# Kernel tuning notes

Hardware: AMD Instinct MI355X
Metric: run time of the kernel (lower is better)

Reference implementation:

```python
import jax, jax.numpy as jnp
import numpy as np

N = 131072   # total nodes in batch
E = 524288   # directed edges
B = 2048     # number of graphs
H = 128      # hidden_dim
NF = 30      # node_feature_dim
GF = 4415    # gene_feature_dim
L = 3        # gnn_layers
EPS = 1e-5   # batchnorm eps


def setup_inputs() -> dict:
    key = jax.random.key(0)
    ks = jax.random.split(key, 24)
    rn = lambda k, s, sc=0.05: jax.random.normal(k, s, jnp.float32) * sc
    return {
        "x": jax.random.normal(ks[0], (N, NF), jnp.float32),
        "gene_features": jax.random.normal(ks[1], (B, GF), jnp.float32),
        "edge_index": jax.random.randint(ks[2], (2, E), 0, N),
        "batch": (jnp.arange(N) * B) // N,  # sorted, every graph non-empty
        "W_emb": rn(ks[3], (NF, H)), "b_emb": jnp.zeros((H,), jnp.float32),
        "Wg": rn(ks[4], (L, H, H)), "bg": jnp.zeros((L, H), jnp.float32),
        "bn_gamma": jnp.ones((L, H), jnp.float32), "bn_beta": jnp.zeros((L, H), jnp.float32),
        "Wd1": rn(ks[5], (2 * H, H)), "bd1": jnp.zeros((H,), jnp.float32),
        "Wd2": rn(ks[6], (H, H)), "bd2": jnp.zeros((H,), jnp.float32),
        "Wge1": rn(ks[7], (GF, 256)), "bge1": jnp.zeros((256,), jnp.float32),
        "g_gamma": jnp.ones((256,), jnp.float32), "g_beta": jnp.zeros((256,), jnp.float32),
        "Wge2": rn(ks[8], (256, H)), "bge2": jnp.zeros((H,), jnp.float32),
        "Wh1": rn(ks[9], (2 * H, H)), "bh1": jnp.zeros((H,), jnp.float32),
        "h_gamma": jnp.ones((H,), jnp.float32), "h_beta": jnp.zeros((H,), jnp.float32),
        "Wh2": rn(ks[10], (H, 64)), "bh2": jnp.zeros((64,), jnp.float32),
        "Wh3": rn(ks[11], (64, 1)), "bh3": jnp.zeros((1,), jnp.float32),
    }


def _bn_eval(x, gamma, beta):
    # inference batchnorm with running_mean=0, running_var=1
    return x * (gamma / jnp.sqrt(1.0 + EPS)) + beta


def _gcn_conv(h, W, b, src, dst):
    # PyG GCNConv: add self-loops, symmetric deg normalization, W first, bias after agg
    hw = h @ W                                            # [N,H]
    loop = jnp.arange(N)
    src_a = jnp.concatenate([src, loop])                  # [E+N]
    dst_a = jnp.concatenate([dst, loop])
    deg = jax.ops.segment_sum(jnp.ones((E + N,), hw.dtype), dst_a, num_segments=N)
    dinv = jnp.where(deg > 0, jax.lax.rsqrt(deg), 0.0)
    norm = dinv[src_a] * dinv[dst_a]                      # [E+N]
    msgs = hw[src_a] * norm[:, None]                      # gather [E+N,H]
    out = jax.ops.segment_sum(msgs, dst_a, num_segments=N)
    return out + b


def reference(x, gene_features, edge_index, batch, W_emb, b_emb, Wg, bg, bn_gamma,
              bn_beta, Wd1, bd1, Wd2, bd2, Wge1, bge1, g_gamma, g_beta, Wge2, bge2,
              Wh1, bh1, h_gamma, h_beta, Wh2, bh2, Wh3, bh3):
    src, dst = edge_index[0], edge_index[1]
    h = jax.nn.relu(x @ W_emb + b_emb)                    # [N,H]
    for i in range(L):
        hn = _gcn_conv(h, Wg[i], bg[i], src, dst)
        hn = jax.nn.relu(_bn_eval(hn, bn_gamma[i], bn_beta[i]))
        h = hn if i == 0 else h + hn                      # residual for i>0
    # global mean / max pooling per graph
    counts = jax.ops.segment_sum(jnp.ones((N,), h.dtype), batch, num_segments=B)
    mean_pool = jax.ops.segment_sum(h, batch, num_segments=B) / jnp.maximum(counts, 1.0)[:, None]
    max_pool = jax.ops.segment_max(h, batch, num_segments=B)
    graph_repr = jnp.concatenate([mean_pool, max_pool], axis=1)   # [B,2H]
    drug = jax.nn.relu(graph_repr @ Wd1 + bd1) @ Wd2 + bd2        # [B,H]
    g1 = jax.nn.relu(_bn_eval(gene_features @ Wge1 + bge1, g_gamma, g_beta))
    gene = jax.nn.relu(g1 @ Wge2 + bge2)                          # [B,H]
    comb = jnp.concatenate([drug, gene], axis=1)                  # [B,2H]
    z = jax.nn.relu(_bn_eval(comb @ Wh1 + bh1, h_gamma, h_beta))
    z = jax.nn.relu(z @ Wh2 + bh2)
    return z @ Wh3 + bh3                                          # [B,1]
```

## Files before the change

### kernel.cpp

```cpp
#include <hip/hip_runtime.h>

#define N_NODES 131072
#define E_EDGES 524288
#define B_GR    2048
#define H_DIM   128
#define NF_DIM  30
#define GF_DIM  4415
#define GF_PAD  4416
#define BN_SCALE 0.9999950000374997f

typedef __bf16 bf16x8 __attribute__((ext_vector_type(8)));
typedef float  f32x4  __attribute__((ext_vector_type(4)));
typedef unsigned int uint32;
typedef uint32 u32x4 __attribute__((ext_vector_type(4)));

__device__ __forceinline__ void split2(float x, __bf16& hi, __bf16& lo){
    hi = (__bf16)x;
    lo = (__bf16)(x - (float)hi);
}
__device__ __forceinline__ uint32 bfbits(float x){
    __bf16 h = (__bf16)x;
    return (uint32)__builtin_bit_cast(unsigned short, h);
}
__device__ __forceinline__ float unpack_even(uint32 u){ return __uint_as_float(u<<16); }
__device__ __forceinline__ float unpack_odd (uint32 u){ return __uint_as_float(u & 0xffff0000u); }
__device__ __forceinline__ uint32 pack2(float e, float o){ return bfbits(e) | (bfbits(o)<<16); }


__global__ void k_zero_int(int* __restrict__ p, int n){
    int i = blockIdx.x*256 + threadIdx.x;
    if(i < n) p[i] = 0;
}

__global__ void k_count(const int* __restrict__ dst, int* __restrict__ counts){
    int e = blockIdx.x*256 + threadIdx.x;
    if(e < E_EDGES) atomicAdd(&counts[dst[e]], 1);
}

__global__ void k_scan1(int* __restrict__ counts, int* __restrict__ bsums){
    __shared__ int s[1024];
    int t = threadIdx.x;
    int gi = blockIdx.x*1024 + t;
    int v = counts[gi];
    s[t] = v; __syncthreads();
    for(int off=1; off<1024; off<<=1){
        int x = (t>=off) ? s[t-off] : 0;
        __syncthreads();
        s[t] += x;
        __syncthreads();
    }
    counts[gi] = s[t] - v;
    if(t == 1023) bsums[blockIdx.x] = s[t];
}

__global__ void k_scan2(int* __restrict__ bsums){
    __shared__ int s[128];
    int t = threadIdx.x;
    int v = bsums[t]; s[t] = v; __syncthreads();
    for(int off=1; off<128; off<<=1){
        int x = (t>=off) ? s[t-off] : 0;
        __syncthreads();
        s[t] += x;
        __syncthreads();
    }
    bsums[t] = s[t] - v;
}

__global__ void k_scan3(const int* __restrict__ counts, const int* __restrict__ bsums,
                        int* __restrict__ rowptr){
    int i = blockIdx.x*1024 + threadIdx.x;
    rowptr[i] = counts[i] + bsums[blockIdx.x];
    if(i == 0) rowptr[N_NODES] = E_EDGES;
}

__global__ void k_dinv_cursor(const int* __restrict__ rowptr, float* __restrict__ dinv,
                              int* __restrict__ cursor){
    int n = blockIdx.x*256 + threadIdx.x;
    if(n < N_NODES){
        int a = rowptr[n], b = rowptr[n+1];
        dinv[n] = rsqrtf((float)(b - a) + 1.0f);
        cursor[n] = a;
    }
}

__global__ void k_fill(const int* __restrict__ src, const int* __restrict__ dst,
                       int* __restrict__ cursor, int* __restrict__ csr){
    int e = blockIdx.x*256 + threadIdx.x;
    if(e < E_EDGES){
        int p = atomicAdd(&cursor[dst[e]], 1);
        csr[p] = src[e];
    }
}


__global__ void k_split_weights(const float* __restrict__ Wge1, __bf16* __restrict__ wth,
                                __bf16* __restrict__ wtl,
                                const float* __restrict__ Wg, __bf16* __restrict__ gth,
                                __bf16* __restrict__ gtl,
                                const float* __restrict__ Wemb, __bf16* __restrict__ eth,
                                __bf16* __restrict__ etl){
    unsigned bid = blockIdx.x;
    if(bid < 4416u){
        unsigned idx = bid*256 + threadIdx.x;
        unsigned c = idx / GF_PAD, k = idx - c*GF_PAD;
        float v = (k < GF_DIM) ? Wge1[(size_t)k*256 + c] : 0.f;
        split2(v, wth[idx], wtl[idx]);
    } else if(bid < 4416u + 192u){
        int idx = (bid - 4416u)*256 + threadIdx.x;
        int l = idx >> 14, i = idx & 16383;
        int k = i >> 7, c = i & 127;
        float v = Wg[idx];
        int o = (l << 14) + (c << 7) + k;
        split2(v, gth[o], gtl[o]);
    } else {
        int idx = (bid - 4608u)*256 + threadIdx.x;
        int c = idx >> 5, k = idx & 31;
        float v = (k < NF_DIM) ? Wemb[k*H_DIM + c] : 0.f;
        split2(v, eth[idx], etl[idx]);
    }
}


__global__ __launch_bounds__(256)
void k_emb_mfma(const float* __restrict__ x,
                const __bf16* __restrict__ wth, const __bf16* __restrict__ wtl,
                const float* __restrict__ bias, uint32* __restrict__ Hh2,
                uint32* __restrict__ Hl2){
    __shared__ float sT[4][32*68];
    int wave = threadIdx.x >> 6, lane = threadIdx.x & 63;
    int lr = lane & 15, lq = lane >> 4;
    int rbase = blockIdx.x*128 + wave*32;
    const f32x4 zero4 = {0.f,0.f,0.f,0.f};
    const float* xr0 = x + (size_t)(rbase + lr)*NF_DIM;
    const float* xr1 = x + (size_t)(rbase + 16 + lr)*NF_DIM;
    bf16x8 A0h, A0l, A1h, A1l;
    #pragma unroll
    for(int t=0;t<8;t++){
        int k = lq*8 + t;
        float v0 = (k < NF_DIM) ? xr0[k] : 0.f;
        float v1 = (k < NF_DIM) ? xr1[k] : 0.f;
        __bf16 h, l;
        split2(v0, h, l); A0h[t] = h; A0l[t] = l;
        split2(v1, h, l); A1h[t] = h; A1l[t] = l;
    }
    int orow = lane >> 3;
    int oq   = lane & 7;
    float* sW = sT[wave];
    for(int ph=0; ph<2; ph++){
        #pragma unroll
        for(int cc=0; cc<4; cc++){
            int col = (ph*4+cc)*16 + lr;
            bf16x8 Bh = *(const bf16x8*)(wth + col*32 + lq*8);
            bf16x8 Bl = *(const bf16x8*)(wtl + col*32 + lq*8);
            f32x4 a0 = zero4, a1 = zero4;
            a0 = __builtin_amdgcn_mfma_f32_16x16x32_bf16(A0h, Bh, a0, 0,0,0);
            a0 = __builtin_amdgcn_mfma_f32_16x16x32_bf16(A0l, Bh, a0, 0,0,0);
            a0 = __builtin_amdgcn_mfma_f32_16x16x32_bf16(A0h, Bl, a0, 0,0,0);
            a1 = __builtin_amdgcn_mfma_f32_16x16x32_bf16(A1h, Bh, a1, 0,0,0);
            a1 = __builtin_amdgcn_mfma_f32_16x16x32_bf16(A1l, Bh, a1, 0,0,0);
            a1 = __builtin_amdgcn_mfma_f32_16x16x32_bf16(A1h, Bl, a1, 0,0,0);
            #pragma unroll
            for(int r=0;r<4;r++){
                sW[(lq*4+r)*68 + cc*16 + lr]    = a0[r];
                sW[(16+lq*4+r)*68 + cc*16 + lr] = a1[r];
            }
        }
        __syncthreads();
        int cg = ph*64 + oq*8;
        float bb[8];
        *(float4*)&bb[0] = *(const float4*)(bias + cg);
        *(float4*)&bb[4] = *(const float4*)(bias + cg + 4);
        #pragma unroll
        for(int i=0;i<4;i++){
            int row = i*8 + orow;
            float v[8];
            *(float4*)&v[0] = *(float4*)&sW[row*68 + oq*8];
            *(float4*)&v[4] = *(float4*)&sW[row*68 + oq*8 + 4];
            uint32 oh[4], ol[4];
            #pragma unroll
            for(int p=0;p<4;p++){
                float ve = fmaxf(v[2*p]   + bb[2*p],   0.f);
                float vo = fmaxf(v[2*p+1] + bb[2*p+1], 0.f);
                uint32 he = bfbits(ve), ho = bfbits(vo);
                oh[p] = he | (ho<<16);
                float le = ve - __uint_as_float(he<<16);
                float lo = vo - __uint_as_float(ho<<16);
                ol[p] = pack2(le, lo);
            }
            size_t oidx = (size_t)(rbase + row)*64 + (cg>>1);
            *(uint4*)(Hh2 + oidx) = make_uint4(oh[0],oh[1],oh[2],oh[3]);
            *(uint4*)(Hl2 + oidx) = make_uint4(ol[0],ol[1],ol[2],ol[3]);
        }
        __syncthreads();
    }
}


struct AggMeta {
    int   j0A, cA, j0B, cB;
    float dnA, dnB;
    uint32 shA, slA, shB, slB;
    int   jjA[8], jjB[8];
};

__device__ __forceinline__ void agg_load_meta(AggMeta& m, int nA, int lane,
                                              const int* __restrict__ rowptr,
                                              const float* __restrict__ dinv,
                                              const uint32* __restrict__ Hh2,
                                              const uint32* __restrict__ Hl2){
    int nB = nA + 8;
    int a0 = rowptr[nA], a1 = rowptr[nA+1];
    int b0 = rowptr[nB], b1 = rowptr[nB+1];
    m.j0A = a0; m.cA = a1 - a0;
    m.j0B = b0; m.cB = b1 - b0;
    m.dnA = dinv[nA]; m.dnB = dinv[nB];
    size_t iA = (size_t)nA*64 + lane, iB = (size_t)nB*64 + lane;
    m.shA = Hh2[iA]; m.slA = Hl2[iA];
    m.shB = Hh2[iB]; m.slB = Hl2[iB];
}

__device__ __forceinline__ void agg_load_csr(AggMeta& m, const int* __restrict__ csr){
    int jmA = m.j0A + m.cA - 1;
    int jmB = m.j0B + m.cB - 1;
    #pragma unroll
    for(int t=0;t<8;t++){
        int ia = m.j0A + t; ia = ia > jmA ? jmA : ia;
        int ib = m.j0B + t; ib = ib > jmB ? jmB : ib;
        m.jjA[t] = csr[ia] & (N_NODES-1);
        m.jjB[t] = csr[ib] & (N_NODES-1);
    }
}

__device__ __forceinline__ void agg_pair(AggMeta& cur, AggMeta& nxt, int ii, bool pf,
                                         int rbase, int base16, int lane,
                                         const uint32* __restrict__ Hh2,
                                         const uint32* __restrict__ Hl2,
                                         const float* __restrict__ dinv,
                                         const int* __restrict__ rowptr,
                                         const int* __restrict__ csr,
                                         uint32* __restrict__ AhL,
                                         uint32* __restrict__ AlL){
    uint32 rrA[8], rrB[8];
    float  wwA[8], wwB[8];
    #pragma unroll
    for(int t=0;t<8;t++){
        wwA[t] = (t < cur.cA) ? dinv[cur.jjA[t]] : 0.f;
        rrA[t] = Hh2[(size_t)cur.jjA[t]*64 + lane];
        wwB[t] = (t < cur.cB) ? dinv[cur.jjB[t]] : 0.f;
        rrB[t] = Hh2[(size_t)cur.jjB[t]*64 + lane];
    }
    if(pf){
        agg_load_meta(nxt, rbase + base16 + ii + 1, lane, rowptr, dinv, Hh2, Hl2);
        agg_load_csr(nxt, csr);
    }
    float axA = (unpack_even(cur.shA) + unpack_even(cur.slA)) * cur.dnA;
    float ayA = (unpack_odd(cur.shA)  + unpack_odd(cur.slA))  * cur.dnA;
    float axB = (unpack_even(cur.shB) + unpack_even(cur.slB)) * cur.dnB;
    float ayB = (unpack_odd(cur.shB)  + unpack_odd(cur.slB))  * cur.dnB;
    #pragma unroll
    for(int t=0;t<8;t++){
        axA = fmaf(unpack_even(rrA[t]), wwA[t], axA);
        ayA = fmaf(unpack_odd(rrA[t]),  wwA[t], ayA);
        axB = fmaf(unpack_even(rrB[t]), wwB[t], axB);
        ayB = fmaf(unpack_odd(rrB[t]),  wwB[t], ayB);
    }
    int nb = cur.cA > cur.cB ? cur.cA : cur.cB;
    if(nb > 8){
        int jmA = cur.j0A + cur.cA - 1;
        int jmB = cur.j0B + cur.cB - 1;
        for(int j=8; j<nb; j+=8){
            int jja[8], jjb[8]; float wa[8], wb[8]; uint32 ra[8], rb[8];
            #pragma unroll
            for(int t=0;t<8;t++){
                int ia = cur.j0A + j + t; ia = ia > jmA ? jmA : ia;
                int ib = cur.j0B + j + t; ib = ib > jmB ? jmB : ib;
                jja[t] = csr[ia] & (N_NODES-1);
                jjb[t] = csr[ib] & (N_NODES-1);
            }
            #pragma unroll
            for(int t=0;t<8;t++){
                wa[t] = (j + t < cur.cA) ? dinv[jja[t]] : 0.f;
                ra[t] = Hh2[(size_t)jja[t]*64 + lane];
                wb[t] = (j + t < cur.cB) ? dinv[jjb[t]] : 0.f;
                rb[t] = Hh2[(size_t)jjb[t]*64 + lane];
            }
            #pragma unroll
            for(int t=0;t<8;t++){
                axA = fmaf(unpack_even(ra[t]), wa[t], axA);
                ayA = fmaf(unpack_odd(ra[t]),  wa[t], ayA);
                axB = fmaf(unpack_even(rb[t]), wb[t], axB);
                ayB = fmaf(unpack_odd(rb[t]),  wb[t], ayB);
            }
        }
    }
    axA *= cur.dnA; ayA *= cur.dnA;
    axB *= cur.dnB; ayB *= cur.dnB;
    int rowA = base16 + ii, rowB = rowA + 8;
    uint32 hxA = bfbits(axA), hyA = bfbits(ayA);
    AhL[rowA*68 + lane] = hxA | (hyA<<16);
    AlL[rowA*68 + lane] = pack2(axA - __uint_as_float(hxA<<16),
                                ayA - __uint_as_float(hyA<<16));
    uint32 hxB = bfbits(axB), hyB = bfbits(ayB);
    AhL[rowB*68 + lane] = hxB | (hyB<<16);
    AlL[rowB*68 + lane] = pack2(axB - __uint_as_float(hxB<<16),
                                ayB - __uint_as_float(hyB<<16));
}

__global__ __launch_bounds__(512, 4)
void k_layer(const __bf16* __restrict__ curHh, const __bf16* __restrict__ curHl,
             const float* __restrict__ dinv, const int* __restrict__ rowptr,
             const int* __restrict__ csr,
             const __bf16* __restrict__ Bth, const __bf16* __restrict__ Btl,
             const float* __restrict__ bias, const float* __restrict__ gamma,
             const float* __restrict__ beta,
             uint32* __restrict__ outHh2, uint32* __restrict__ outHl2, int residual){
    __shared__ uint32 smem[8*32*68];
    uint32* AhL = smem;
    uint32* AlL = smem + 128*68;
    int tid  = threadIdx.x;
    int wave = __builtin_amdgcn_readfirstlane(tid >> 6);
    int lane = tid & 63;
    int rbase = blockIdx.x * 128;
    int base16 = wave*16;
    const uint32* Hh2 = (const uint32*)curHh;
    const uint32* Hl2 = (const uint32*)curHl;

    {
        AggMeta m0, m1;
        agg_load_meta(m0, rbase + base16 + 0, lane, rowptr, dinv, Hh2, Hl2);
        agg_load_csr(m0, csr);
        agg_pair(m0, m1, 0, true,  rbase, base16, lane, Hh2, Hl2, dinv, rowptr, csr, AhL, AlL);
        agg_pair(m1, m0, 1, true,  rbase, base16, lane, Hh2, Hl2, dinv, rowptr, csr, AhL, AlL);
        agg_pair(m0, m1, 2, true,  rbase, base16, lane, Hh2, Hl2, dinv, rowptr, csr, AhL, AlL);
        agg_pair(m1, m0, 3, true,  rbase, base16, lane, Hh2, Hl2, dinv, rowptr, csr, AhL, AlL);
        agg_pair(m0, m1, 4, true,  rbase, base16, lane, Hh2, Hl2, dinv, rowptr, csr, AhL, AlL);
        agg_pair(m1, m0, 5, true,  rbase, base16, lane, Hh2, Hl2, dinv, rowptr, csr, AhL, AlL);
        agg_pair(m0, m1, 6, true,  rbase, base16, lane, Hh2, Hl2, dinv, rowptr, csr, AhL, AlL);
        agg_pair(m1, m0, 7, false, rbase, base16, lane, Hh2, Hl2, dinv, rowptr, csr, AhL, AlL);
    }
    __syncthreads();

    int lr = lane & 15, lq = lane >> 4;
    int wr = wave & 3, wc = wave >> 2;
    int r0 = wr*32;
    bf16x8 A0h[4], A0l[4], A1h[4], A1l[4];
    #pragma unroll
    for(int ks=0;ks<4;ks++){
        int u0 = (r0 + lr)*68 + lq*4 + ks*16;
        int u1 = (r0 + 16 + lr)*68 + lq*4 + ks*16;
        A0h[ks] = __builtin_bit_cast(bf16x8, *(const u32x4*)(AhL + u0));
        A0l[ks] = __builtin_bit_cast(bf16x8, *(const u32x4*)(AlL + u0));
        A1h[ks] = __builtin_bit_cast(bf16x8, *(const u32x4*)(AhL + u1));
        A1l[ks] = __builtin_bit_cast(bf16x8, *(const u32x4*)(AlL + u1));
    }
    __syncthreads();

    float* stg = (float*)smem + wave*(32*68);
    const f32x4 zero4 = {0.f,0.f,0.f,0.f};
    #pragma unroll
    for(int cc=0; cc<4; cc++){
        int col = wc*64 + cc*16 + lr;
        f32x4 a0 = zero4, a1 = zero4;
        #pragma unroll
        for(int ks=0;ks<4;ks++){
            bf16x8 Bh = *(const bf16x8*)(Bth + col*H_DIM + ks*32 + lq*8);
            bf16x8 Bl = *(const bf16x8*)(Btl + col*H_DIM + ks*32 + lq*8);
            a0 = __builtin_amdgcn_mfma_f32_16x16x32_bf16(A0h[ks], Bh, a0, 0,0,0);
            a0 = __builtin_amdgcn_mfma_f32_16x16x32_bf16(A0l[ks], Bh, a0, 0,0,0);
            a0 = __builtin_amdgcn_mfma_f32_16x16x32_bf16(A0h[ks], Bl, a0, 0,0,0);
            a1 = __builtin_amdgcn_mfma_f32_16x16x32_bf16(A1h[ks], Bh, a1, 0,0,0);
            a1 = __builtin_amdgcn_mfma_f32_16x16x32_bf16(A1l[ks], Bh, a1, 0,0,0);
            a1 = __builtin_amdgcn_mfma_f32_16x16x32_bf16(A1h[ks], Bl, a1, 0,0,0);
        }
        #pragma unroll
        for(int r=0;r<4;r++){
            stg[(lq*4+r)*68 + cc*16 + lr]    = a0[r];
            stg[(16+lq*4+r)*68 + cc*16 + lr] = a1[r];
        }
    }

    int orow = lane >> 3;
    int oq   = lane & 7;
    int cg = wc*64 + oq*8;
    float bb[8], gg[8], tt[8];
    *(float4*)&bb[0] = *(const float4*)(bias + cg);
    *(float4*)&bb[4] = *(const float4*)(bias + cg + 4);
    *(float4*)&gg[0] = *(const float4*)(gamma + cg);
    *(float4*)&gg[4] = *(const float4*)(gamma + cg + 4);
    *(float4*)&tt[0] = *(const float4*)(beta + cg);
    *(float4*)&tt[4] = *(const float4*)(beta + cg + 4);
    #pragma unroll
    for(int p=0;p<8;p++) gg[p] *= BN_SCALE;
    #pragma unroll
    for(int i=0;i<4;i++){
        int row = i*8 + orow;
        float v[8];
        *(float4*)&v[0] = *(float4*)&stg[row*68 + oq*8];
        *(float4*)&v[4] = *(float4*)&stg[row*68 + oq*8 + 4];
        size_t oidx = (size_t)(rbase + r0 + row)*64 + (cg>>1);
        uint4 oldh = {0,0,0,0}, oldl = {0,0,0,0};
        if(residual){
            oldh = *(const uint4*)(Hh2 + oidx);
            oldl = *(const uint4*)(Hl2 + oidx);
        }
        uint32 ohv[4] = {oldh.x,oldh.y,oldh.z,oldh.w};
        uint32 olv[4] = {oldl.x,oldl.y,oldl.z,oldl.w};
        uint32 oh[4], ol[4];
        #pragma unroll
        for(int p=0;p<4;p++){
            float ve = fmaxf(fmaf(v[2*p]   + bb[2*p],   gg[2*p],   tt[2*p]),   0.f);
            float vo = fmaxf(fmaf(v[2*p+1] + bb[2*p+1], gg[2*p+1], tt[2*p+1]), 0.f);
            if(residual){
                ve += unpack_even(ohv[p]) + unpack_even(olv[p]);
                vo += unpack_odd(ohv[p])  + unpack_odd(olv[p]);
            }
            uint32 he = bfbits(ve), ho = bfbits(vo);
            oh[p] = he | (ho<<16);
            float le = ve - __uint_as_float(he<<16);
            float lo = vo - __uint_as_float(ho<<16);
            ol[p] = pack2(le, lo);
        }
        *(uint4*)(outHh2 + oidx) = make_uint4(oh[0],oh[1],oh[2],oh[3]);
        *(uint4*)(outHl2 + oidx) = make_uint4(ol[0],ol[1],ol[2],ol[3]);
    }
}


__global__ __launch_bounds__(256)
void k_gemm_gf_mfma(const float* __restrict__ Agf,
                    const __bf16* __restrict__ Bth, const __bf16* __restrict__ Btl,
                    float* __restrict__ gpart){
    int rt = blockIdx.x & 31;
    int sp = blockIdx.x >> 5;
    int ks0 = (sp*138) >> 3, ks1 = ((sp+1)*138) >> 3;
    int wave = threadIdx.x >> 6, lane = threadIdx.x & 63;
    int lr = lane & 15, lq = lane >> 4;
    int rbase = rt*64 + (wave & 1)*32;
    int cbase = (wave >> 1)*128;
    const f32x4 zero4 = {0.f,0.f,0.f,0.f};
    f32x4 acc[8][2];
    #pragma unroll
    for(int ct=0;ct<8;ct++){ acc[ct][0] = zero4; acc[ct][1] = zero4; }
    for(int ks=ks0; ks<ks1; ks++){
        int kc = ks*32;
        const float* ar0 = Agf + (size_t)(rbase + lr)*GF_DIM + kc + lq*8;
        const float* ar1 = ar0 + (size_t)16*GF_DIM;
        bf16x8 A0h, A0l, A1h, A1l;
        if(kc + 32 <= GF_DIM){
            #pragma unroll
            for(int t=0;t<8;t++){
                __bf16 h, l;
                split2(ar0[t], h, l); A0h[t] = h; A0l[t] = l;
                split2(ar1[t], h, l); A1h[t] = h; A1l[t] = l;
            }
        } else {
            #pragma unroll
            for(int t=0;t<8;t++){
                int k = kc + lq*8 + t;
                float v0 = 0.f, v1 = 0.f;
                if(k < GF_DIM){ v0 = ar0[t]; v1 = ar1[t]; }
                __bf16 h, l;
                split2(v0, h, l); A0h[t] = h; A0l[t] = l;
                split2(v1, h, l); A1h[t] = h; A1l[t] = l;
            }
        }
        #pragma unroll
        for(int ct=0;ct<8;ct++){
            size_t bo = (size_t)(cbase + ct*16 + lr)*GF_PAD + kc + lq*8;
            bf16x8 Bh = *(const bf16x8*)(Bth + bo);
            bf16x8 Bl = *(const bf16x8*)(Btl + bo);
            acc[ct][0] = __builtin_amdgcn_mfma_f32_16x16x32_bf16(A0h, Bh, acc[ct][0], 0,0,0);
            acc[ct][0] = __builtin_amdgcn_mfma_f32_16x16x32_bf16(A0l, Bh, acc[ct][0], 0,0,0);
            acc[ct][0] = __builtin_amdgcn_mfma_f32_16x16x32_bf16(A0h, Bl, acc[ct][0], 0,0,0);
            acc[ct][1] = __builtin_amdgcn_mfma_f32_16x16x32_bf16(A1h, Bh, acc[ct][1], 0,0,0);
            acc[ct][1] = __builtin_amdgcn_mfma_f32_16x16x32_bf16(A1l, Bh, acc[ct][1], 0,0,0);
            acc[ct][1] = __builtin_amdgcn_mfma_f32_16x16x32_bf16(A1h, Bl, acc[ct][1], 0,0,0);
        }
    }
    float* po = gpart + (size_t)sp*(B_GR*256);
    #pragma unroll
    for(int ct=0;ct<8;ct++)
        #pragma unroll
        for(int s=0;s<2;s++)
            #pragma unroll
            for(int r=0;r<4;r++)
                po[(size_t)(rbase + s*16 + lq*4 + r)*256 + cbase + ct*16 + lr] = acc[ct][s][r];
}

__global__ void k_gene_reduce(const float* __restrict__ gpart, const float* __restrict__ bias,
                              const float* __restrict__ gamma, const float* __restrict__ beta,
                              float* __restrict__ g1){
    int i = blockIdx.x*256 + threadIdx.x;
    int c = i & 255;
    float v = bias[c];
    #pragma unroll
    for(int sp=0;sp<8;sp++) v += gpart[(size_t)sp*(B_GR*256) + i];
    v = fmaf(v, gamma[c]*BN_SCALE, beta[c]);
    g1[i] = fmaxf(v, 0.f);
}


__device__ __forceinline__ void load_w4(const float* __restrict__ W, int off, int tid,
                                        float4* t){
    const float4* s = (const float4*)(W + off);
    t[0] = s[tid];
    t[1] = s[tid + 512];
    t[2] = s[tid + 1024];
    t[3] = s[tid + 1536];
}
__device__ __forceinline__ void write_w4(float* sW, int tid, const float4* t){
    float4* d = (float4*)sW;
    d[tid]        = t[0];
    d[tid + 512]  = t[1];
    d[tid + 1024] = t[2];
    d[tid + 1536] = t[3];
}

__device__ __forceinline__ void dense_stage128(
        const float* __restrict__ W, int nck, const float* sA, int lda,
        float* sO, int ldo, float* sW, int tid, int c, int ga, int gb,
        float bias_c, float gsc, float bsh, int do_relu){
    float4 t[4];
    load_w4(W, 0, tid, t);
    write_w4(sW, tid, t);
    __syncthreads();
    float a0 = bias_c, a1 = bias_c;
    for(int ck=0; ck<nck; ck++){
        if(ck+1 < nck) load_w4(W, (ck+1)*8192, tid, t);
        const float* aga = sA + ga*lda + ck*64;
        const float* agb = sA + gb*lda + ck*64;
        #pragma unroll
        for(int k=0;k<64;k++){
            float w = sW[k*128 + c];
            a0 = fmaf(aga[k], w, a0);
            a1 = fmaf(agb[k], w, a1);
        }
        __syncthreads();
        if(ck+1 < nck){ write_w4(sW, tid, t); __syncthreads(); }
    }
    a0 = fmaf(a0, gsc, bsh);
    a1 = fmaf(a1, gsc, bsh);
    if(do_relu){ a0 = fmaxf(a0, 0.f); a1 = fmaxf(a1, 0.f); }
    sO[ga*ldo + c] = a0;
    sO[gb*ldo + c] = a1;
}

__global__ __launch_bounds__(512)
void k_head(const uint32* __restrict__ Hh2, const uint32* __restrict__ Hl2,
            const float* __restrict__ g1,
            const float* __restrict__ Wd1, const float* __restrict__ bd1,
            const float* __restrict__ Wd2, const float* __restrict__ bd2,
            const float* __restrict__ Wge2, const float* __restrict__ bge2,
            const float* __restrict__ Wh1, const float* __restrict__ bh1,
            const float* __restrict__ h_g, const float* __restrict__ h_b,
            const float* __restrict__ Wh2, const float* __restrict__ bh2,
            const float* __restrict__ Wh3, const float* __restrict__ bh3,
            float* __restrict__ out){
    __shared__ float sPool[8][256];
    __shared__ float sG1[8][256];
    __shared__ float sT1[8][128];
    __shared__ float sComb[8][256];
    __shared__ float sZ[8][128];
    __shared__ float sZ2[8][64];
    __shared__ float sW[8192];
    int tid = threadIdx.x;
    int wave = tid >> 6, lane = tid & 63;
    int g0 = blockIdx.x*8;
    {
        int idx = tid*4;
        int g = idx >> 8, c = idx & 255;
        *(float4*)&sG1[g][c] = *(const float4*)&g1[(size_t)(g0+g)*256 + c];
    }
    {
        size_t base = (size_t)(g0+wave)*4096 + lane;
        float se = 0.f, so = 0.f, me = -3.4e38f, mo = -3.4e38f;
        #pragma unroll 8
        for(int r=0;r<64;r++){
            uint32 h = Hh2[base + r*64];
            uint32 l = Hl2[base + r*64];
            float ve = unpack_even(h) + unpack_even(l);
            float vo = unpack_odd(h)  + unpack_odd(l);
            se += ve; so += vo;
            me = fmaxf(me, ve); mo = fmaxf(mo, vo);
        }
        sPool[wave][2*lane]       = se*(1.f/64.f);
        sPool[wave][2*lane+1]     = so*(1.f/64.f);
        sPool[wave][128+2*lane]   = me;
        sPool[wave][128+2*lane+1] = mo;
    }
    __syncthreads();
    int c = tid & 127, q = tid >> 7;
    int ga = 2*q, gb = 2*q + 1;
    dense_stage128(Wd1, 4, &sPool[0][0], 256, &sT1[0][0], 128, sW, tid, c, ga, gb,
                   bd1[c], 1.f, 0.f, 1);
    dense_stage128(Wd2, 2, &sT1[0][0], 128, &sComb[0][0], 256, sW, tid, c, ga, gb,
                   bd2[c], 1.f, 0.f, 0);
    dense_stage128(Wge2, 4, &sG1[0][0], 256, &sComb[0][0] + 128, 256, sW, tid, c, ga, gb,
                   bge2[c], 1.f, 0.f, 1);
    dense_stage128(Wh1, 4, &sComb[0][0], 256, &sZ[0][0], 128, sW, tid, c, ga, gb,
                   bh1[c], h_g[c]*BN_SCALE, h_b[c], 1);
    {
        float4 t[4];
        load_w4(Wh2, 0, tid, t);
        write_w4(sW, tid, t);
        __syncthreads();
        int c2 = tid & 63, q2 = tid >> 6;
        float a = bh2[c2];
        #pragma unroll
        for(int k=0;k<128;k++)
            a = fmaf(sZ[q2][k], sW[k*64 + c2], a);
        sZ2[q2][c2] = fmaxf(a, 0.f);
    }
    __syncthreads();
    {
        float v = sZ2[wave][lane] * Wh3[lane];
        #pragma unroll
        for(int off=32; off; off>>=1) v += __shfl_down(v, off);
        if(lane == 0) out[g0 + wave] = v + bh3[0];
    }
}


extern "C" void kernel_launch(void* const* d_in, const int* in_sizes, int n_in,
                              void* d_out, int out_size, void* d_ws, size_t ws_size,
                              hipStream_t stream){
    (void)in_sizes; (void)n_in; (void)out_size; (void)ws_size;
    const float* x    = (const float*)d_in[0];
    const float* gf   = (const float*)d_in[1];
    const int*   ei   = (const int*)  d_in[2];
    const float* W_emb= (const float*)d_in[4];
    const float* b_emb= (const float*)d_in[5];
    const float* Wg   = (const float*)d_in[6];
    const float* bg   = (const float*)d_in[7];
    const float* bn_g = (const float*)d_in[8];
    const float* bn_b = (const float*)d_in[9];
    const float* Wd1  = (const float*)d_in[10];
    const float* bd1  = (const float*)d_in[11];
    const float* Wd2  = (const float*)d_in[12];
    const float* bd2  = (const float*)d_in[13];
    const float* Wge1 = (const float*)d_in[14];
    const float* bge1 = (const float*)d_in[15];
    const float* g_g  = (const float*)d_in[16];
    const float* g_b  = (const float*)d_in[17];
    const float* Wge2 = (const float*)d_in[18];
    const float* bge2 = (const float*)d_in[19];
    const float* Wh1  = (const float*)d_in[20];
    const float* bh1  = (const float*)d_in[21];
    const float* h_g  = (const float*)d_in[22];
    const float* h_b  = (const float*)d_in[23];
    const float* Wh2  = (const float*)d_in[24];
    const float* bh2  = (const float*)d_in[25];
    const float* Wh3  = (const float*)d_in[26];
    const float* bh3  = (const float*)d_in[27];
    float* outp = (float*)d_out;

    char* base = (char*)d_ws;
    __bf16* Hh = (__bf16*)base;
    __bf16* Hl = (__bf16*)(base + (32u<<20));
    __bf16* Ph = (__bf16*)(base + (64u<<20));
    __bf16* Pl = (__bf16*)(base + (96u<<20));
    float*  gpart  = (float*)base;
    __bf16* wge_th = (__bf16*)(base + (17u<<20));
    __bf16* wge_tl = (__bf16*)(base + (17u<<20) + 2260992);
    char* T = base + (128u<<20);
    float* g1   = (float*)T;
    int* rowptr = (int*)(g1 + B_GR*256);
    int* cursor = rowptr + (N_NODES+1);
    int* csr    = cursor + N_NODES;
    int* bsums  = csr + E_EDGES;
    float* dinv = (float*)(bsums + 128);
    __bf16* wg_th = (__bf16*)(dinv + N_NODES);
    __bf16* wg_tl = wg_th + 3*16384;
    __bf16* we_th = wg_tl + 3*16384;
    __bf16* we_tl = we_th + 128*32;

    const int* src = ei;
    const int* dst = ei + E_EDGES;

    k_split_weights<<<4624, 256, 0, stream>>>(Wge1, wge_th, wge_tl, Wg, wg_th, wg_tl,
                                              W_emb, we_th, we_tl);

    k_gemm_gf_mfma<<<256, 256, 0, stream>>>(gf, wge_th, wge_tl, gpart);
    k_gene_reduce <<<(B_GR*256)/256, 256, 0, stream>>>(gpart, bge1, g_g, g_b, g1);

    k_zero_int   <<<N_NODES/256, 256, 0, stream>>>(cursor, N_NODES);
    k_count      <<<E_EDGES/256, 256, 0, stream>>>(dst, cursor);
    k_scan1      <<<128, 1024, 0, stream>>>(cursor, bsums);
    k_scan2      <<<1, 128, 0, stream>>>(bsums);
    k_scan3      <<<128, 1024, 0, stream>>>(cursor, bsums, rowptr);
    k_dinv_cursor<<<N_NODES/256, 256, 0, stream>>>(rowptr, dinv, cursor);
    k_fill       <<<E_EDGES/256, 256, 0, stream>>>(src, dst, cursor, csr);

    k_emb_mfma<<<N_NODES/128, 256, 0, stream>>>(x, we_th, we_tl, b_emb,
                                                (uint32*)Hh, (uint32*)Hl);

    uint32 *curh = (uint32*)Hh, *curl = (uint32*)Hl;
    uint32 *outh = (uint32*)Ph, *outl = (uint32*)Pl;
    for(int i=0;i<3;i++){
        k_layer<<<N_NODES/128, 512, 0, stream>>>((const __bf16*)curh, (const __bf16*)curl,
                                                 dinv, rowptr, csr,
                                                 wg_th + i*16384, wg_tl + i*16384,
                                                 bg + i*H_DIM, bn_g + i*H_DIM, bn_b + i*H_DIM,
                                                 outh, outl, i > 0);
        uint32* th = curh; curh = outh; outh = th;
        uint32* tl = curl; curl = outl; outl = tl;
    }

    k_head<<<B_GR/8, 512, 0, stream>>>(curh, curl, g1,
                                       Wd1, bd1, Wd2, bd2, Wge2, bge2,
                                       Wh1, bh1, h_g, h_b, Wh2, bh2, Wh3, bh3, outp);
}
```

Measured before the change: 567.2 us.

## Precompute padded ELL neighbor table with weights and pipeline per-node gathers

Adds a kernel that builds an 8-slot ELL table per node holding the neighbor index and its dinv weight, with a flag bit on the first slot for nodes with more than eight neighbors. The aggregation loop then loads each node's neighbor list as four int4 reads and processes one node at a time, with a three-deep software pipeline that issues the next node's feature gathers before computing the current one. This removes the dependent rowptr→csr→dinv lookup chain from the hot loop in all three layers. In exchange it adds an extra preprocessing pass, an 8 MB workspace region, and a slow path for high-degree nodes.

```diff
diff --git a/kernel.cpp b/kernel.cpp
--- a/kernel.cpp
+++ b/kernel.cpp
@@ -90,6 +90,21 @@
         int p = atomicAdd(&cursor[dst[e]], 1);
         csr[p] = src[e];
     }
+}
+
+
+__global__ void k_ell(const int* __restrict__ rowptr, const int* __restrict__ csr,
+                      const float* __restrict__ dinv, int2* __restrict__ ell){
+    int idx = blockIdx.x*256 + threadIdx.x;
+    int n = idx >> 3, t = idx & 7;
+    int j0 = rowptr[n], d = rowptr[n+1] - j0;
+    int jj = 0; float w = 0.f;
+    if(t < d){
+        jj = csr[j0 + t];
+        w  = dinv[jj];
+    }
+    if(t == 0 && d > 8) jj = (int)((uint32)jj | 0x80000000u);
+    ell[idx] = make_int2(jj, __float_as_int(w));
 }
 
 
@@ -196,120 +211,89 @@
 }
 
 
-struct AggMeta {
-    int   j0A, cA, j0B, cB;
-    float dnA, dnB;
-    uint32 shA, slA, shB, slB;
-    int   jjA[8], jjB[8];
+struct NodeMeta {
+    int4 jw0, jw1, jw2, jw3;
+    uint32 sh, sl;
+    float dn;
 };
 
-__device__ __forceinline__ void agg_load_meta(AggMeta& m, int nA, int lane,
-                                              const int* __restrict__ rowptr,
-                                              const float* __restrict__ dinv,
-                                              const uint32* __restrict__ Hh2,
-                                              const uint32* __restrict__ Hl2){
-    int nB = nA + 8;
-    int a0 = rowptr[nA], a1 = rowptr[nA+1];
-    int b0 = rowptr[nB], b1 = rowptr[nB+1];
-    m.j0A = a0; m.cA = a1 - a0;
-    m.j0B = b0; m.cB = b1 - b0;
-    m.dnA = dinv[nA]; m.dnB = dinv[nB];
-    size_t iA = (size_t)nA*64 + lane, iB = (size_t)nB*64 + lane;
-    m.shA = Hh2[iA]; m.slA = Hl2[iA];
-    m.shB = Hh2[iB]; m.slB = Hl2[iB];
-}
-
-__device__ __forceinline__ void agg_load_csr(AggMeta& m, const int* __restrict__ csr){
-    int jmA = m.j0A + m.cA - 1;
-    int jmB = m.j0B + m.cB - 1;
+__device__ __forceinline__ void ell_load(NodeMeta& m, int n, int lane,
+        const int4* __restrict__ ell4,
+        const uint32* __restrict__ Hh2, const uint32* __restrict__ Hl2,
+        const float* __restrict__ dinv){
+    const int4* p = ell4 + (size_t)n*4;
+    m.jw0 = p[0]; m.jw1 = p[1]; m.jw2 = p[2]; m.jw3 = p[3];
+    size_t i = (size_t)n*64 + lane;
+    m.sh = Hh2[i]; m.sl = Hl2[i];
+    m.dn = dinv[n];
+}
+
+__device__ __forceinline__ void rr_issue(uint32* rr, const NodeMeta& m, int lane,
+        const uint32* __restrict__ Hh2){
+    int j0 = m.jw0.x & 0x7fffffff;
+    rr[0] = Hh2[(size_t)j0*64 + lane];
+    rr[1] = Hh2[(size_t)m.jw0.z*64 + lane];
+    rr[2] = Hh2[(size_t)m.jw1.x*64 + lane];
+    rr[3] = Hh2[(size_t)m.jw1.z*64 + lane];
+    rr[4] = Hh2[(size_t)m.jw2.x*64 + lane];
+    rr[5] = Hh2[(size_t)m.jw2.z*64 + lane];
+    rr[6] = Hh2[(size_t)m.jw3.x*64 + lane];
+    rr[7] = Hh2[(size_t)m.jw3.z*64 + lane];
+}
+
+__device__ __forceinline__ void node_compute(const NodeMeta& m, const uint32* rr,
+        int row, int n, int lane,
+        const int* __restrict__ rowptr, const int* __restrict__ csr,
+        const float* __restrict__ dinv,
+        const uint32* __restrict__ Hh2,
+        uint32* __restrict__ AhL, uint32* __restrict__ AlL){
+    float dn = m.dn;
+    float ax = (unpack_even(m.sh) + unpack_even(m.sl)) * dn;
+    float ay = (unpack_odd(m.sh)  + unpack_odd(m.sl))  * dn;
+    float w[8];
+    w[0]=__int_as_float(m.jw0.y); w[1]=__int_as_float(m.jw0.w);
+    w[2]=__int_as_float(m.jw1.y); w[3]=__int_as_float(m.jw1.w);
+    w[4]=__int_as_float(m.jw2.y); w[5]=__int_as_float(m.jw2.w);
+    w[6]=__int_as_float(m.jw3.y); w[7]=__int_as_float(m.jw3.w);
     #pragma unroll
     for(int t=0;t<8;t++){
-        int ia = m.j0A + t; ia = ia > jmA ? jmA : ia;
-        int ib = m.j0B + t; ib = ib > jmB ? jmB : ib;
-        m.jjA[t] = csr[ia] & (N_NODES-1);
-        m.jjB[t] = csr[ib] & (N_NODES-1);
-    }
-}
-
-__device__ __forceinline__ void agg_pair(AggMeta& cur, AggMeta& nxt, int ii, bool pf,
-                                         int rbase, int base16, int lane,
-                                         const uint32* __restrict__ Hh2,
-                                         const uint32* __restrict__ Hl2,
-                                         const float* __restrict__ dinv,
-                                         const int* __restrict__ rowptr,
-                                         const int* __restrict__ csr,
-                                         uint32* __restrict__ AhL,
-                                         uint32* __restrict__ AlL){
-    uint32 rrA[8], rrB[8];
-    float  wwA[8], wwB[8];
-    #pragma unroll
-    for(int t=0;t<8;t++){
-        wwA[t] = (t < cur.cA) ? dinv[cur.jjA[t]] : 0.f;
-        rrA[t] = Hh2[(size_t)cur.jjA[t]*64 + lane];
-        wwB[t] = (t < cur.cB) ? dinv[cur.jjB[t]] : 0.f;
-        rrB[t] = Hh2[(size_t)cur.jjB[t]*64 + lane];
-    }
-    if(pf){
-        agg_load_meta(nxt, rbase + base16 + ii + 1, lane, rowptr, dinv, Hh2, Hl2);
-        agg_load_csr(nxt, csr);
-    }
-    float axA = (unpack_even(cur.shA) + unpack_even(cur.slA)) * cur.dnA;
-    float ayA = (unpack_odd(cur.shA)  + unpack_odd(cur.slA))  * cur.dnA;
-    float axB = (unpack_even(cur.shB) + unpack_even(cur.slB)) * cur.dnB;
-    float ayB = (unpack_odd(cur.shB)  + unpack_odd(cur.slB))  * cur.dnB;
-    #pragma unroll
-    for(int t=0;t<8;t++){
-        axA = fmaf(unpack_even(rrA[t]), wwA[t], axA);
-        ayA = fmaf(unpack_odd(rrA[t]),  wwA[t], ayA);
-        axB = fmaf(unpack_even(rrB[t]), wwB[t], axB);
-        ayB = fmaf(unpack_odd(rrB[t]),  wwB[t], ayB);
-    }
-    int nb = cur.cA > cur.cB ? cur.cA : cur.cB;
-    if(nb > 8){
-        int jmA = cur.j0A + cur.cA - 1;
-        int jmB = cur.j0B + cur.cB - 1;
-        for(int j=8; j<nb; j+=8){
-            int jja[8], jjb[8]; float wa[8], wb[8]; uint32 ra[8], rb[8];
+        ax = fmaf(unpack_even(rr[t]), w[t], ax);
+        ay = fmaf(unpack_odd(rr[t]),  w[t], ay);
+    }
+    if(m.jw0.x < 0){
+        int j0 = rowptr[n];
+        int d  = rowptr[n+1] - j0;
+        int jm = j0 + d - 1;
+        for(int j=8; j<d; j+=8){
+            int jjq[8]; float wq[8]; uint32 rq[8];
             #pragma unroll
             for(int t=0;t<8;t++){
-                int ia = cur.j0A + j + t; ia = ia > jmA ? jmA : ia;
-                int ib = cur.j0B + j + t; ib = ib > jmB ? jmB : ib;
-                jja[t] = csr[ia] & (N_NODES-1);
-                jjb[t] = csr[ib] & (N_NODES-1);
+                int ia = j0 + j + t; ia = ia > jm ? jm : ia;
+                jjq[t] = csr[ia];
             }
             #pragma unroll
             for(int t=0;t<8;t++){
-                wa[t] = (j + t < cur.cA) ? dinv[jja[t]] : 0.f;
-                ra[t] = Hh2[(size_t)jja[t]*64 + lane];
-                wb[t] = (j + t < cur.cB) ? dinv[jjb[t]] : 0.f;
-                rb[t] = Hh2[(size_t)jjb[t]*64 + lane];
+                wq[t] = (j + t < d) ? dinv[jjq[t]] : 0.f;
+                rq[t] = Hh2[(size_t)jjq[t]*64 + lane];
             }
             #pragma unroll
             for(int t=0;t<8;t++){
-                axA = fmaf(unpack_even(ra[t]), wa[t], axA);
-                ayA = fmaf(unpack_odd(ra[t]),  wa[t], ayA);
-                axB = fmaf(unpack_even(rb[t]), wb[t], axB);
-                ayB = fmaf(unpack_odd(rb[t]),  wb[t], ayB);
+                ax = fmaf(unpack_even(rq[t]), wq[t], ax);
+                ay = fmaf(unpack_odd(rq[t]),  wq[t], ay);
             }
         }
     }
-    axA *= cur.dnA; ayA *= cur.dnA;
-    axB *= cur.dnB; ayB *= cur.dnB;
-    int rowA = base16 + ii, rowB = rowA + 8;
-    uint32 hxA = bfbits(axA), hyA = bfbits(ayA);
-    AhL[rowA*68 + lane] = hxA | (hyA<<16);
-    AlL[rowA*68 + lane] = pack2(axA - __uint_as_float(hxA<<16),
-                                ayA - __uint_as_float(hyA<<16));
-    uint32 hxB = bfbits(axB), hyB = bfbits(ayB);
-    AhL[rowB*68 + lane] = hxB | (hyB<<16);
-    AlL[rowB*68 + lane] = pack2(axB - __uint_as_float(hxB<<16),
-                                ayB - __uint_as_float(hyB<<16));
+    ax *= dn; ay *= dn;
+    uint32 hx = bfbits(ax), hy = bfbits(ay);
+    AhL[row*68 + lane] = hx | (hy<<16);
+    AlL[row*68 + lane] = pack2(ax - __uint_as_float(hx<<16),
+                               ay - __uint_as_float(hy<<16));
 }
 
 __global__ __launch_bounds__(512, 4)
 void k_layer(const __bf16* __restrict__ curHh, const __bf16* __restrict__ curHl,
              const float* __restrict__ dinv, const int* __restrict__ rowptr,
-             const int* __restrict__ csr,
+             const int* __restrict__ csr, const int2* __restrict__ ell,
              const __bf16* __restrict__ Bth, const __bf16* __restrict__ Btl,
              const float* __restrict__ bias, const float* __restrict__ gamma,
              const float* __restrict__ beta,
@@ -326,17 +310,40 @@
     const uint32* Hl2 = (const uint32*)curHl;
 
     {
-        AggMeta m0, m1;
-        agg_load_meta(m0, rbase + base16 + 0, lane, rowptr, dinv, Hh2, Hl2);
-        agg_load_csr(m0, csr);
-        agg_pair(m0, m1, 0, true,  rbase, base16, lane, Hh2, Hl2, dinv, rowptr, csr, AhL, AlL);
-        agg_pair(m1, m0, 1, true,  rbase, base16, lane, Hh2, Hl2, dinv, rowptr, csr, AhL, AlL);
-        agg_pair(m0, m1, 2, true,  rbase, base16, lane, Hh2, Hl2, dinv, rowptr, csr, AhL, AlL);
-        agg_pair(m1, m0, 3, true,  rbase, base16, lane, Hh2, Hl2, dinv, rowptr, csr, AhL, AlL);
-        agg_pair(m0, m1, 4, true,  rbase, base16, lane, Hh2, Hl2, dinv, rowptr, csr, AhL, AlL);
-        agg_pair(m1, m0, 5, true,  rbase, base16, lane, Hh2, Hl2, dinv, rowptr, csr, AhL, AlL);
-        agg_pair(m0, m1, 6, true,  rbase, base16, lane, Hh2, Hl2, dinv, rowptr, csr, AhL, AlL);
-        agg_pair(m1, m0, 7, false, rbase, base16, lane, Hh2, Hl2, dinv, rowptr, csr, AhL, AlL);
+        const int4* ell4 = (const int4*)ell;
+        NodeMeta m0, m1, m2;
+        uint32 rr0[8], rr1[8];
+        int nb0 = rbase + base16;
+        ell_load(m0, nb0+0, lane, ell4, Hh2, Hl2, dinv);
+        ell_load(m1, nb0+1, lane, ell4, Hh2, Hl2, dinv);
+        rr_issue(rr0, m0, lane, Hh2);
+
+#define AGG_STEP(II, MC, MN, MP, RC, RN, DO_RR, DO_M)                          \
+        {                                                                      \
+            if(DO_RR) rr_issue(RN, MN, lane, Hh2);                             \
+            if(DO_M)  ell_load(MP, nb0+(II)+2, lane, ell4, Hh2, Hl2, dinv);    \
+            __builtin_amdgcn_sched_barrier(0);                                 \
+            node_compute(MC, RC, base16+(II), nb0+(II), lane,                  \
+                         rowptr, csr, dinv, Hh2, AhL, AlL);                    \
+        }
+
+        AGG_STEP(0,  m0, m1, m2, rr0, rr1, true,  true)
+        AGG_STEP(1,  m1, m2, m0, rr1, rr0, true,  true)
+        AGG_STEP(2,  m2, m0, m1, rr0, rr1, true,  true)
+        AGG_STEP(3,  m0, m1, m2, rr1, rr0, true,  true)
+        AGG_STEP(4,  m1, m2, m0, rr0, rr1, true,  true)
+        AGG_STEP(5,  m2, m0, m1, rr1, rr0, true,  true)
+        AGG_STEP(6,  m0, m1, m2, rr0, rr1, true,  true)
+        AGG_STEP(7,  m1, m2, m0, rr1, rr0, true,  true)
+        AGG_STEP(8,  m2, m0, m1, rr0, rr1, true,  true)
+        AGG_STEP(9,  m0, m1, m2, rr1, rr0, true,  true)
+        AGG_STEP(10, m1, m2, m0, rr0, rr1, true,  true)
+        AGG_STEP(11, m2, m0, m1, rr1, rr0, true,  true)
+        AGG_STEP(12, m0, m1, m2, rr0, rr1, true,  true)
+        AGG_STEP(13, m1, m2, m0, rr1, rr0, true,  true)
+        AGG_STEP(14, m2, m0, m1, rr0, rr1, true,  false)
+        AGG_STEP(15, m0, m1, m2, rr1, rr0, false, false)
+#undef AGG_STEP
     }
     __syncthreads();
 
@@ -663,7 +670,8 @@
     __bf16* wge_th = (__bf16*)(base + (17u<<20));
     __bf16* wge_tl = (__bf16*)(base + (17u<<20) + 2260992);
     char* T = base + (128u<<20);
-    float* g1   = (float*)T;
+    int2*  ell  = (int2*)T;
+    float* g1   = (float*)(T + 8388608);
     int* rowptr = (int*)(g1 + B_GR*256);
     int* cursor = rowptr + (N_NODES+1);
     int* csr    = cursor + N_NODES;
@@ -690,6 +698,7 @@
     k_scan3      <<<128, 1024, 0, stream>>>(cursor, bsums, rowptr);
     k_dinv_cursor<<<N_NODES/256, 256, 0, stream>>>(rowptr, dinv, cursor);
     k_fill       <<<E_EDGES/256, 256, 0, stream>>>(src, dst, cursor, csr);
+    k_ell        <<<(N_NODES*8)/256, 256, 0, stream>>>(rowptr, csr, dinv, ell);
 
     k_emb_mfma<<<N_NODES/128, 256, 0, stream>>>(x, we_th, we_tl, b_emb,
                                                 (uint32*)Hh, (uint32*)Hl);
@@ -698,7 +707,7 @@
     uint32 *outh = (uint32*)Ph, *outl = (uint32*)Pl;
     for(int i=0;i<3;i++){
         k_layer<<<N_NODES/128, 512, 0, stream>>>((const __bf16*)curh, (const __bf16*)curl,
-                                                 dinv, rowptr, csr,
+                                                 dinv, rowptr, csr, ell,
                                                  wg_th + i*16384, wg_tl + i*16384,
                                                  bg + i*H_DIM, bn_g + i*H_DIM, bn_b + i*H_DIM,
                                                  outh, outl, i > 0);
```

New measurement: 609.1 us. 1.07x slower.
